# Optimization experiments

Hardware: AMD Instinct MI355X
Metric: run time of the kernel (lower is better)

The kernel has to match this reference:

```python
import jax, jax.numpy as jnp
import numpy as np
import math

D_MODEL = 128
N_HEADS = 8
D_FF = 512
FACTOR = 3
EPS = 1e-5


def _ln(x, g, b):
    mu = x.mean(-1, keepdims=True)
    var = ((x - mu) ** 2).mean(-1, keepdims=True)
    return (x - mu) / jnp.sqrt(var + EPS) * g + b


def setup_inputs() -> dict:
    key = jax.random.key(0)
    ks = jax.random.split(key, 16)
    d, dff = D_MODEL, D_FF
    s = 0.02
    return {
        "x": jax.random.normal(ks[0], (4, 32, 256), dtype=jnp.float32),
        "mlp_w": jax.random.normal(ks[1], (d,)) * s,  # Conv2d(1,d,1x1) weight squeezed
        "mlp_b": jnp.zeros((d,), jnp.float32),
        "wq": jax.random.normal(ks[2], (d, d)) * s, "bq": jnp.zeros((d,), jnp.float32),
        "wk": jax.random.normal(ks[3], (d, d)) * s, "bk": jnp.zeros((d,), jnp.float32),
        "wv": jax.random.normal(ks[4], (d, d)) * s, "bv": jnp.zeros((d,), jnp.float32),
        "wo": jax.random.normal(ks[5], (d, d)) * s, "bo": jnp.zeros((d,), jnp.float32),
        "w1": jax.random.normal(ks[6], (dff, d)) * s, "b1": jnp.zeros((dff,), jnp.float32),
        "w2": jax.random.normal(ks[7], (d, dff)) * s, "b2": jnp.zeros((d,), jnp.float32),
        "ln1_g": jnp.ones((d,), jnp.float32), "ln1_b": jnp.zeros((d,), jnp.float32),
        "ln2_g": jnp.ones((d,), jnp.float32), "ln2_b": jnp.zeros((d,), jnp.float32),
    }


def reference(x, mlp_w, mlp_b, wq, bq, wk, bk, wv, bv, wo, bo,
              w1, b1, w2, b2, ln1_g, ln1_b, ln2_g, ln2_b):
    b, N, T = x.shape
    C, H = D_MODEL, N_HEADS
    E = C // H
    # 1x1 Conv2d from 1 channel -> per-channel affine of scalar input
    h = x[..., None] * mlp_w + mlp_b                      # [b,N,T,C]
    h = h.reshape(b * N, T, C)                            # [B,L,C]
    B, L = h.shape[0], T
    q = (h @ wq.T + bq).reshape(B, L, H, E).transpose(0, 2, 1, 3)  # [B,H,L,E]
    k = (h @ wk.T + bk).reshape(B, L, H, E).transpose(0, 2, 1, 3)
    v = (h @ wv.T + bv).reshape(B, L, H, E).transpose(0, 2, 1, 3)

    sample_k = min(FACTOR * math.ceil(math.log(L)), L)
    u = min(FACTOR * math.ceil(math.log(L)), L)
    # random K-sample indices shared across batch/heads (torch.randint analogue)
    idx = jax.random.randint(jax.random.key(42), (L, sample_k), 0, L)

    scores_full = jnp.einsum('bhle,bhse->bhls', q, k)     # [B,H,L,L]
    qk_sample = jnp.take_along_axis(scores_full, idx[None, None], axis=-1)  # [B,H,L,sample_k]
    M = qk_sample.max(-1) - qk_sample.sum(-1) / L         # sparsity measure
    m_top = jax.lax.top_k(M, u)[1]                        # [B,H,u] top-u query indices
    scores_top = jnp.take_along_axis(scores_full, m_top[..., None], axis=2)  # [B,H,u,L]
    scores_top = scores_top / math.sqrt(E)

    attn = jax.nn.softmax(scores_top, axis=-1)
    upd = jnp.einsum('bhul,bhle->bhue', attn, v)          # [B,H,u,E]
    # mask_flag=False: initial context = mean(V) broadcast over queries
    context = jnp.broadcast_to(v.mean(axis=2, keepdims=True), v.shape)
    bi = jnp.arange(B)[:, None, None]
    hi = jnp.arange(H)[None, :, None]
    context = context.at[bi, hi, m_top].set(upd)          # scatter top-u updates

    out = context.transpose(0, 2, 1, 3).reshape(B, L, C) @ wo.T + bo
    x1 = _ln(h + out, ln1_g, ln1_b)
    y = jax.nn.relu(x1 @ w1.T + b1) @ w2.T + b2           # 1x1 conv1d pair == MLP
    out2 = _ln(x1 + y, ln2_g, ln2_b)
    out2 = out2.reshape(b, N, T, C).sum(axis=1)           # sum over N
    return out2.transpose(0, 2, 1)                        # [b,C,T]
```

## Files before the change

### kernel.cpp

```cpp
#include <hip/hip_runtime.h>
#include <stdint.h>
#include <math.h>


#define EPSF 1e-5f

typedef short bf16x8 __attribute__((ext_vector_type(8)));
typedef float f32x4  __attribute__((ext_vector_type(4)));

__device__ __forceinline__ unsigned short f2bf(float f) {
  union { float f; unsigned u; } v; v.f = f;
  unsigned r = v.u + 0x7FFFu + ((v.u >> 16) & 1u);
  return (unsigned short)(r >> 16);
}
__device__ __forceinline__ float bf2f(unsigned short u) {
  union { unsigned u; float f; } v; v.u = ((unsigned)u) << 16;
  return v.f;
}
__device__ __forceinline__ float waveSum(float v) {
  #pragma unroll
  for (int m = 32; m > 0; m >>= 1) v += __shfl_xor(v, m);
  return v;
}

__device__ __forceinline__ void threefry2x32_k42(uint32_t& x0, uint32_t& x1) {
  const uint32_t ks0 = 0u, ks1 = 42u, ks2 = 0u ^ 42u ^ 0x1BD11BDAu;
  x0 += ks0; x1 += ks1;
#define TF_R(d) { x0 += x1; x1 = (x1 << d) | (x1 >> (32 - d)); x1 ^= x0; }
  TF_R(13) TF_R(15) TF_R(26) TF_R(6)  x0 += ks1; x1 += ks2 + 1u;
  TF_R(17) TF_R(29) TF_R(16) TF_R(24) x0 += ks2; x1 += ks0 + 2u;
  TF_R(13) TF_R(15) TF_R(26) TF_R(6)  x0 += ks0; x1 += ks1 + 3u;
  TF_R(17) TF_R(29) TF_R(16) TF_R(24) x0 += ks1; x1 += ks2 + 4u;
  TF_R(13) TF_R(15) TF_R(26) TF_R(6)  x0 += ks2; x1 += ks0 + 5u;
#undef TF_R
}

__global__ __launch_bounds__(256) void setup_kernel(
    const float* __restrict__ mlp_w, const float* __restrict__ mlp_b,
    const float* __restrict__ wq, const float* __restrict__ bq,
    const float* __restrict__ wk, const float* __restrict__ bk,
    const float* __restrict__ wv, const float* __restrict__ bv,
    const float* __restrict__ wo, const float* __restrict__ bo,
    const float* __restrict__ w1, const float* __restrict__ w2,
    int* __restrict__ idxT, float* __restrict__ cst,
    unsigned short* __restrict__ w1bf, unsigned short* __restrict__ w2bf) {
  int tid = threadIdx.x;
  {
    int gid = blockIdx.x * 256 + tid;
    int base = gid * 16;
    const float* src; unsigned short* dst; int off;
    if (base < 65536) { src = w1; dst = w1bf; off = base; }
    else              { src = w2; dst = w2bf; off = base - 65536; }
    #pragma unroll 4
    for (int k = 0; k < 16; k++) dst[off + k] = f2bf(src[off + k]);
  }
  if (blockIdx.x != 0) return;
  for (int p = tid; p < 2304; p += 256) {
    uint32_t a = (uint32_t)p, bb = (uint32_t)(p + 2304);
    threefry2x32_k42(a, bb);
    int l0 = p / 18, j0 = p - l0 * 18;
    int p2 = p + 2304;
    int l1 = p2 / 18, j1 = p2 - l1 * 18;
    idxT[j0 * 256 + l0] = (int)(a & 0xFFu);
    idxT[j1 * 256 + l1] = (int)(bb & 0xFFu);
  }
  if (tid < 128) {
    float aq = 0.f, cq_ = 0.f, ak = 0.f, ck_ = 0.f, av = 0.f, cv_ = 0.f;
    for (int c = 0; c < 128; c++) {
      float w = mlp_w[c], bb = mlp_b[c];
      float q = wq[tid * 128 + c], k = wk[tid * 128 + c], v = wv[tid * 128 + c];
      aq += q * w; cq_ += q * bb;
      ak += k * w; ck_ += k * bb;
      av += v * w; cv_ += v * bb;
    }
    cst[0   + tid] = aq;
    cst[128 + tid] = cq_ + bq[tid];
    cst[256 + tid] = ak;
    cst[384 + tid] = ck_ + bk[tid];
    cst[512 + tid] = av;
    cst[640 + tid] = cv_ + bv[tid];
  }
  __syncthreads();
  if (tid < 8) {
    float a = 0.f, b = 0.f, g = 0.f, d = 0.f;
    for (int e = 0; e < 16; e++) {
      int j = tid * 16 + e;
      float Aq = cst[j], Cq = cst[128 + j], Ak = cst[256 + j], Ck = cst[384 + j];
      a += Aq * Ak; b += Aq * Ck; g += Cq * Ak; d += Cq * Ck;
    }
    cst[768 + tid] = a; cst[776 + tid] = b; cst[784 + tid] = g; cst[792 + tid] = d;
  }
  if (tid < 128) {
    float oc = 0.f;
    for (int h = 0; h < 8; h++) {
      float s = 0.f;
      for (int e = 0; e < 16; e++) {
        float w = wo[tid * 128 + h * 16 + e];
        s  += w * cst[512 + h * 16 + e];
        oc += w * cst[640 + h * 16 + e];
      }
      cst[800 + h * 128 + tid] = s;
    }
    cst[1824 + tid] = oc + bo[tid] + mlp_b[tid];
  }
}

__global__ __launch_bounds__(256) void attn_kernel(
    const float* __restrict__ x, const int* __restrict__ idxT,
    const float* __restrict__ cst, float* __restrict__ g) {
  __shared__ float xr[256];
  __shared__ float Mb[512];
  __shared__ float selv[512];
  __shared__ float rsum[4], rmax[4], rmin[4];
  __shared__ int   items[64];
  __shared__ float witem[64];
  __shared__ int   cnt;
  int tid = threadIdx.x, lane = tid & 63, w = tid >> 6;
  int seq = blockIdx.x >> 2, hg = blockIdx.x & 3;
  if (tid == 0) cnt = 0;
  float xv = x[seq * 256 + tid];
  xr[tid] = xv;
  float s = waveSum(xv);
  float mx = xv, mn = xv;
  #pragma unroll
  for (int m = 32; m > 0; m >>= 1) {
    mx = fmaxf(mx, __shfl_xor(mx, m));
    mn = fminf(mn, __shfl_xor(mn, m));
  }
  if (lane == 0) { rsum[w] = s; rmax[w] = mx; rmin[w] = mn; }
  __syncthreads();
  float meanx = (rsum[0] + rsum[1] + rsum[2] + rsum[3]) * (1.0f / 256.0f);
  float maxx = fmaxf(fmaxf(rmax[0], rmax[1]), fmaxf(rmax[2], rmax[3]));
  float minx = fminf(fminf(rmin[0], rmin[1]), fminf(rmin[2], rmin[3]));
  float mx18 = -INFINITY, mn18 = INFINITY, s18 = 0.f;
  #pragma unroll 3
  for (int j = 0; j < 18; j++) {
    float xs = xr[idxT[j * 256 + tid]];
    mx18 = fmaxf(mx18, xs); mn18 = fminf(mn18, xs); s18 += xs;
  }
  int h0 = hg * 2, h1 = h0 + 1;
  float al0 = cst[768 + h0], be0 = cst[776 + h0], ga0 = cst[784 + h0], de0 = cst[792 + h0];
  float al1 = cst[768 + h1], be1 = cst[776 + h1], ga1 = cst[784 + h1], de1 = cst[792 + h1];
  float ac0 = fmaf(al0, xv, ga0), cc0 = fmaf(be0, xv, de0);
  float ac1 = fmaf(al1, xv, ga1), cc1 = fmaf(be1, xv, de1);
  float M0 = ((ac0 >= 0.f ? ac0 * mx18 : ac0 * mn18) + cc0)
           - (fmaf(ac0, s18, 18.f * cc0)) * (1.0f / 256.0f);
  float M1 = ((ac1 >= 0.f ? ac1 * mx18 : ac1 * mn18) + cc1)
           - (fmaf(ac1, s18, 18.f * cc1)) * (1.0f / 256.0f);
  Mb[tid] = M0; Mb[256 + tid] = M1;
  __syncthreads();
  int r0 = 0, r1 = 0;
  #pragma unroll 4
  for (int j = 0; j < 256; j++) {
    float a = Mb[j], bb = Mb[256 + j];
    r0 += (a > M0) || (a == M0 && j < tid);
    r1 += (bb > M1) || (bb == M1 && j < tid);
  }
  selv[tid] = meanx; selv[256 + tid] = meanx;
  if (r0 < 18) { int p = atomicAdd(&cnt, 1); items[p] = tid;       witem[p] = 0.25f * ac0; }
  if (r1 < 18) { int p = atomicAdd(&cnt, 1); items[p] = 256 + tid; witem[p] = 0.25f * ac1; }
  __syncthreads();
  int nIt = cnt;
  for (int i = w; i < nIt; i += 4) {
    int it = items[i]; float wv = witem[i];
    float m0 = (wv >= 0.f) ? wv * maxx : wv * minx;
    float S1 = 0.f, Sx = 0.f;
    #pragma unroll
    for (int cch = 0; cch < 4; cch++) {
      float xs = xr[lane + cch * 64];
      float e = __expf(fmaf(wv, xs, -m0));
      S1 += e; Sx = fmaf(xs, e, Sx);
    }
    #pragma unroll
    for (int m = 32; m > 0; m >>= 1) {
      S1 += __shfl_xor(S1, m); Sx += __shfl_xor(Sx, m);
    }
    if (lane == 0) selv[it] = Sx / S1;
  }
  __syncthreads();
  float2 gv; gv.x = selv[tid]; gv.y = selv[256 + tid];
  *(float2*)&g[(size_t)((seq << 8) + tid) * 8 + hg * 2] = gv;
}

__global__ __launch_bounds__(256) void mega_kernel(
    const float* __restrict__ x, const float* __restrict__ g,
    const float* __restrict__ cst, const float* __restrict__ mlp_w,
    const unsigned short* __restrict__ w1bf, const float* __restrict__ b1,
    const unsigned short* __restrict__ w2bf, const float* __restrict__ b2,
    const float* __restrict__ ln1g, const float* __restrict__ ln1b,
    const float* __restrict__ ln2g, const float* __restrict__ ln2b,
    float* __restrict__ out) {
  __shared__ unsigned short x1s[64 * 136];
  __shared__ unsigned short a1s[64 * 264];
  __shared__ float partial[512];
  int tid = threadIdx.x, lane = tid & 63, w = tid >> 6;
  int col = lane & 15, quad = lane >> 4;
  int b = blockIdx.x >> 7, t0 = (blockIdx.x & 127) << 1;

  {
    int c0 = lane << 1;
    float mwa = mlp_w[c0], mwb = mlp_w[c0 | 1];
    float cca = cst[1824 + c0], ccb = cst[1824 + (c0 | 1)];
    float wva[8], wvb[8];
    #pragma unroll
    for (int h = 0; h < 8; h++) {
      wva[h] = cst[800 + h * 128 + c0];
      wvb[h] = cst[800 + h * 128 + (c0 | 1)];
    }
    float g1a = ln1g[c0], g1b = ln1g[c0 | 1];
    float e1a = ln1b[c0], e1b = ln1b[c0 | 1];
    for (int tk = 0; tk < 16; tk++) {
      int row = w * 16 + tk;
      int td = row >> 5, n = row & 31;
      int tok = ((b * 32 + n) << 8) + t0 + td;
      float xvv = x[tok];
      const float* gp = g + (size_t)tok * 8;
      float ra = fmaf(xvv, mwa, cca), rb = fmaf(xvv, mwb, ccb);
      #pragma unroll
      for (int h = 0; h < 8; h++) {
        float gh = gp[h];
        ra = fmaf(gh, wva[h], ra); rb = fmaf(gh, wvb[h], rb);
      }
      float su = waveSum(ra + rb);
      float mu = su * (1.0f / 128.0f);
      float da = ra - mu, db = rb - mu;
      float vs = waveSum(da * da + db * db);
      float inv = rsqrtf(vs * (1.0f / 128.0f) + EPSF);
      unsigned int pa = f2bf(da * inv * g1a + e1a);
      unsigned int pb = f2bf(db * inv * g1b + e1b);
      *(unsigned int*)&x1s[row * 136 + c0] = pa | (pb << 16);
    }
  }
  __syncthreads();

  f32x4 acc2[8];
  #pragma unroll
  for (int i = 0; i < 8; i++) acc2[i] = (f32x4){0.f, 0.f, 0.f, 0.f};

  for (int fh = 0; fh < 2; fh++) {
    f32x4 acc1[16];
    #pragma unroll
    for (int i = 0; i < 16; i++) acc1[i] = (f32x4){0.f, 0.f, 0.f, 0.f};
    #pragma unroll
    for (int ks = 0; ks < 4; ks++) {
      bf16x8 af[4];
      #pragma unroll
      for (int rg = 0; rg < 4; rg++)
        af[rg] = *(const bf16x8*)&x1s[(rg * 16 + col) * 136 + ks * 32 + quad * 8];
      #pragma unroll
      for (int ft = 0; ft < 4; ft++) {
        int f = fh * 256 + w * 64 + ft * 16 + col;
        bf16x8 bf = *(const bf16x8*)(w1bf + f * 128 + ks * 32 + quad * 8);
        #pragma unroll
        for (int rg = 0; rg < 4; rg++)
          acc1[rg * 4 + ft] = __builtin_amdgcn_mfma_f32_16x16x32_bf16(
              af[rg], bf, acc1[rg * 4 + ft], 0, 0, 0);
      }
    }
    if (fh) __syncthreads();
    #pragma unroll
    for (int ft = 0; ft < 4; ft++) {
      int fl = w * 64 + ft * 16 + col;
      float bv = b1[fh * 256 + fl];
      #pragma unroll
      for (int rg = 0; rg < 4; rg++) {
        f32x4 a = acc1[rg * 4 + ft];
        #pragma unroll
        for (int r = 0; r < 4; r++) {
          float vv = fmaxf(a[r] + bv, 0.f);
          a1s[(rg * 16 + quad * 4 + r) * 264 + fl] = f2bf(vv);
        }
      }
    }
    __syncthreads();
    #pragma unroll
    for (int ks = 0; ks < 8; ks++) {
      bf16x8 a2 = *(const bf16x8*)&a1s[(w * 16 + col) * 264 + ks * 32 + quad * 8];
      #pragma unroll
      for (int tc = 0; tc < 8; tc++) {
        int c = tc * 16 + col;
        bf16x8 bf = *(const bf16x8*)(w2bf + c * 512 + fh * 256 + ks * 32 + quad * 8);
        acc2[tc] = __builtin_amdgcn_mfma_f32_16x16x32_bf16(a2, bf, acc2[tc], 0, 0, 0);
      }
    }
  }

  float z[8][4];
  float b2c[8], g2c[8], e2c[8];
  #pragma unroll
  for (int tc = 0; tc < 8; tc++) {
    int c = tc * 16 + col;
    b2c[tc] = b2[c]; g2c[tc] = ln2g[c]; e2c[tc] = ln2b[c];
  }
  #pragma unroll
  for (int tc = 0; tc < 8; tc++)
    #pragma unroll
    for (int r = 0; r < 4; r++) {
      float x1v = bf2f(x1s[(w * 16 + quad * 4 + r) * 136 + tc * 16 + col]);
      z[tc][r] = acc2[tc][r] + b2c[tc] + x1v;
    }
  float mu[4], inv[4];
  #pragma unroll
  for (int r = 0; r < 4; r++) {
    float s = 0.f;
    #pragma unroll
    for (int tc = 0; tc < 8; tc++) s += z[tc][r];
    #pragma unroll
    for (int m = 1; m <= 8; m <<= 1) s += __shfl_xor(s, m);
    mu[r] = s * (1.0f / 128.0f);
  }
  #pragma unroll
  for (int r = 0; r < 4; r++) {
    float q = 0.f;
    #pragma unroll
    for (int tc = 0; tc < 8; tc++) {
      float d = z[tc][r] - mu[r]; q += d * d;
    }
    #pragma unroll
    for (int m = 1; m <= 8; m <<= 1) q += __shfl_xor(q, m);
    inv[r] = rsqrtf(q * (1.0f / 128.0f) + EPSF);
  }
  float nsum[8];
  #pragma unroll
  for (int tc = 0; tc < 8; tc++) {
    float s = 0.f;
    #pragma unroll
    for (int r = 0; r < 4; r++) {
      float o = (z[tc][r] - mu[r]) * inv[r] * g2c[tc] + e2c[tc];
      s += o;
    }
    s += __shfl_xor(s, 16);
    s += __shfl_xor(s, 32);
    nsum[tc] = s;
  }
  if (quad == 0) {
    #pragma unroll
    for (int tc = 0; tc < 8; tc++) partial[w * 128 + tc * 16 + col] = nsum[tc];
  }
  __syncthreads();
  {
    int c = tid & 127, tp = tid >> 7;
    float v = partial[(tp * 2) * 128 + c] + partial[(tp * 2 + 1) * 128 + c];
    out[(size_t)(b * 128 + c) * 256 + t0 + tp] = v;
  }
}

extern "C" void kernel_launch(void* const* d_in, const int* in_sizes, int n_in,
                              void* d_out, int out_size, void* d_ws, size_t ws_size,
                              hipStream_t stream) {
  (void)in_sizes; (void)n_in; (void)out_size; (void)ws_size;
  const float* x    = (const float*)d_in[0];
  const float* mlpw = (const float*)d_in[1];
  const float* mlpb = (const float*)d_in[2];
  const float* wq   = (const float*)d_in[3];
  const float* bq   = (const float*)d_in[4];
  const float* wk   = (const float*)d_in[5];
  const float* bk   = (const float*)d_in[6];
  const float* wv   = (const float*)d_in[7];
  const float* bv   = (const float*)d_in[8];
  const float* wo   = (const float*)d_in[9];
  const float* bo   = (const float*)d_in[10];
  const float* w1   = (const float*)d_in[11];
  const float* b1   = (const float*)d_in[12];
  const float* w2   = (const float*)d_in[13];
  const float* b2   = (const float*)d_in[14];
  const float* ln1g = (const float*)d_in[15];
  const float* ln1b = (const float*)d_in[16];
  const float* ln2g = (const float*)d_in[17];
  const float* ln2b = (const float*)d_in[18];

  char* ws = (char*)d_ws;
  int*            idxT = (int*)(ws);
  float*          cst  = (float*)(ws + 20480);
  unsigned short* w1bf = (unsigned short*)(ws + 32768);
  unsigned short* w2bf = (unsigned short*)(ws + 163840);
  float*          gbuf = (float*)(ws + 294912);
  float*          outp = (float*)d_out;

  hipLaunchKernelGGL(setup_kernel, dim3(32), dim3(256), 0, stream,
                     mlpw, mlpb, wq, bq, wk, bk, wv, bv, wo, bo, w1, w2,
                     idxT, cst, w1bf, w2bf);
  hipLaunchKernelGGL(attn_kernel, dim3(512), dim3(256), 0, stream,
                     x, idxT, cst, gbuf);
  hipLaunchKernelGGL(mega_kernel, dim3(512), dim3(256), 0, stream,
                     x, gbuf, cst, mlpw, w1bf, b1, w2bf, b2,
                     ln1g, ln1b, ln2g, ln2b, outp);
}
```

Measured before the change: 178.5 us.

## Halve mega_kernel tile to 32 rows, restructure LN2 epilogue, refine attn top-k

The MLP mega_kernel now handles one time step (32 rows) per block instead of two, doubling the grid to 1024 blocks. Shared memory is reduced by overlaying a1s with a z buffer, launch bounds request 4 blocks per CU, and the second GEMM is split across waves by output column. LayerNorm2 and the sum over N are redone through shared memory with float4 reads and shuffle reductions. In attn_kernel the rank loop reads Mb as float4, and the softmax pass runs on 32-lane groups using x values preloaded into registers. The extra blocks reload the same weights more often from global memory in exchange for more parallelism and occupancy.

```diff
diff --git a/kernel.cpp b/kernel.cpp
--- a/kernel.cpp
+++ b/kernel.cpp
@@ -132,6 +132,10 @@
   float meanx = (rsum[0] + rsum[1] + rsum[2] + rsum[3]) * (1.0f / 256.0f);
   float maxx = fmaxf(fmaxf(rmax[0], rmax[1]), fmaxf(rmax[2], rmax[3]));
   float minx = fminf(fminf(rmin[0], rmin[1]), fminf(rmin[2], rmin[3]));
+  int l32 = tid & 31, grp = tid >> 5;
+  float xs8[8];
+  #pragma unroll
+  for (int k = 0; k < 8; k++) xs8[k] = xr[l32 + k * 32];
   float mx18 = -INFINITY, mn18 = INFINITY, s18 = 0.f;
   #pragma unroll 3
   for (int j = 0; j < 18; j++) {
@@ -150,39 +154,46 @@
   Mb[tid] = M0; Mb[256 + tid] = M1;
   __syncthreads();
   int r0 = 0, r1 = 0;
+  const float4* Mb4 = (const float4*)Mb;
   #pragma unroll 4
-  for (int j = 0; j < 256; j++) {
-    float a = Mb[j], bb = Mb[256 + j];
-    r0 += (a > M0) || (a == M0 && j < tid);
-    r1 += (bb > M1) || (bb == M1 && j < tid);
+  for (int j4 = 0; j4 < 64; j4++) {
+    float4 a = Mb4[j4], bb = Mb4[64 + j4];
+    int base = j4 * 4;
+    r0 += (a.x > M0) || (a.x == M0 && base     < tid);
+    r0 += (a.y > M0) || (a.y == M0 && base + 1 < tid);
+    r0 += (a.z > M0) || (a.z == M0 && base + 2 < tid);
+    r0 += (a.w > M0) || (a.w == M0 && base + 3 < tid);
+    r1 += (bb.x > M1) || (bb.x == M1 && base     < tid);
+    r1 += (bb.y > M1) || (bb.y == M1 && base + 1 < tid);
+    r1 += (bb.z > M1) || (bb.z == M1 && base + 2 < tid);
+    r1 += (bb.w > M1) || (bb.w == M1 && base + 3 < tid);
   }
   selv[tid] = meanx; selv[256 + tid] = meanx;
   if (r0 < 18) { int p = atomicAdd(&cnt, 1); items[p] = tid;       witem[p] = 0.25f * ac0; }
   if (r1 < 18) { int p = atomicAdd(&cnt, 1); items[p] = 256 + tid; witem[p] = 0.25f * ac1; }
   __syncthreads();
   int nIt = cnt;
-  for (int i = w; i < nIt; i += 4) {
+  for (int i = grp; i < nIt; i += 8) {
     int it = items[i]; float wv = witem[i];
     float m0 = (wv >= 0.f) ? wv * maxx : wv * minx;
     float S1 = 0.f, Sx = 0.f;
     #pragma unroll
-    for (int cch = 0; cch < 4; cch++) {
-      float xs = xr[lane + cch * 64];
-      float e = __expf(fmaf(wv, xs, -m0));
-      S1 += e; Sx = fmaf(xs, e, Sx);
-    }
-    #pragma unroll
-    for (int m = 32; m > 0; m >>= 1) {
+    for (int k = 0; k < 8; k++) {
+      float e = __expf(fmaf(wv, xs8[k], -m0));
+      S1 += e; Sx = fmaf(xs8[k], e, Sx);
+    }
+    #pragma unroll
+    for (int m = 16; m > 0; m >>= 1) {
       S1 += __shfl_xor(S1, m); Sx += __shfl_xor(Sx, m);
     }
-    if (lane == 0) selv[it] = Sx / S1;
+    if (l32 == 0) selv[it] = Sx / S1;
   }
   __syncthreads();
   float2 gv; gv.x = selv[tid]; gv.y = selv[256 + tid];
   *(float2*)&g[(size_t)((seq << 8) + tid) * 8 + hg * 2] = gv;
 }
 
-__global__ __launch_bounds__(256) void mega_kernel(
+__global__ __launch_bounds__(256, 4) void mega_kernel(
     const float* __restrict__ x, const float* __restrict__ g,
     const float* __restrict__ cst, const float* __restrict__ mlp_w,
     const unsigned short* __restrict__ w1bf, const float* __restrict__ b1,
@@ -190,12 +201,14 @@
     const float* __restrict__ ln1g, const float* __restrict__ ln1b,
     const float* __restrict__ ln2g, const float* __restrict__ ln2b,
     float* __restrict__ out) {
-  __shared__ unsigned short x1s[64 * 136];
-  __shared__ unsigned short a1s[64 * 264];
-  __shared__ float partial[512];
+  __shared__ unsigned short x1s[32 * 136];
+  __shared__ char ovl[32 * 264 * 2];
+  __shared__ float psum[512];
+  unsigned short* a1s = (unsigned short*)ovl;
+  float*          zbuf = (float*)ovl;
   int tid = threadIdx.x, lane = tid & 63, w = tid >> 6;
   int col = lane & 15, quad = lane >> 4;
-  int b = blockIdx.x >> 7, t0 = (blockIdx.x & 127) << 1;
+  int b = blockIdx.x >> 8, t = blockIdx.x & 255;
 
   {
     int c0 = lane << 1;
@@ -209,18 +222,21 @@
     }
     float g1a = ln1g[c0], g1b = ln1g[c0 | 1];
     float e1a = ln1b[c0], e1b = ln1b[c0 | 1];
-    for (int tk = 0; tk < 16; tk++) {
-      int row = w * 16 + tk;
-      int td = row >> 5, n = row & 31;
-      int tok = ((b * 32 + n) << 8) + t0 + td;
+    for (int tk = 0; tk < 8; tk++) {
+      int n = w * 8 + tk;
+      int tok = ((b * 32 + n) << 8) + t;
       float xvv = x[tok];
-      const float* gp = g + (size_t)tok * 8;
+      float4 gA = *(const float4*)(g + (size_t)tok * 8);
+      float4 gB = *(const float4*)(g + (size_t)tok * 8 + 4);
       float ra = fmaf(xvv, mwa, cca), rb = fmaf(xvv, mwb, ccb);
-      #pragma unroll
-      for (int h = 0; h < 8; h++) {
-        float gh = gp[h];
-        ra = fmaf(gh, wva[h], ra); rb = fmaf(gh, wvb[h], rb);
-      }
+      ra = fmaf(gA.x, wva[0], ra); rb = fmaf(gA.x, wvb[0], rb);
+      ra = fmaf(gA.y, wva[1], ra); rb = fmaf(gA.y, wvb[1], rb);
+      ra = fmaf(gA.z, wva[2], ra); rb = fmaf(gA.z, wvb[2], rb);
+      ra = fmaf(gA.w, wva[3], ra); rb = fmaf(gA.w, wvb[3], rb);
+      ra = fmaf(gB.x, wva[4], ra); rb = fmaf(gB.x, wvb[4], rb);
+      ra = fmaf(gB.y, wva[5], ra); rb = fmaf(gB.y, wvb[5], rb);
+      ra = fmaf(gB.z, wva[6], ra); rb = fmaf(gB.z, wvb[6], rb);
+      ra = fmaf(gB.w, wva[7], ra); rb = fmaf(gB.w, wvb[7], rb);
       float su = waveSum(ra + rb);
       float mu = su * (1.0f / 128.0f);
       float da = ra - mu, db = rb - mu;
@@ -228,33 +244,33 @@
       float inv = rsqrtf(vs * (1.0f / 128.0f) + EPSF);
       unsigned int pa = f2bf(da * inv * g1a + e1a);
       unsigned int pb = f2bf(db * inv * g1b + e1b);
-      *(unsigned int*)&x1s[row * 136 + c0] = pa | (pb << 16);
-    }
-  }
-  __syncthreads();
-
-  f32x4 acc2[8];
+      *(unsigned int*)&x1s[n * 136 + c0] = pa | (pb << 16);
+    }
+  }
+  __syncthreads();
+
+  f32x4 acc2[4];
   #pragma unroll
-  for (int i = 0; i < 8; i++) acc2[i] = (f32x4){0.f, 0.f, 0.f, 0.f};
+  for (int i = 0; i < 4; i++) acc2[i] = (f32x4){0.f, 0.f, 0.f, 0.f};
 
   for (int fh = 0; fh < 2; fh++) {
-    f32x4 acc1[16];
-    #pragma unroll
-    for (int i = 0; i < 16; i++) acc1[i] = (f32x4){0.f, 0.f, 0.f, 0.f};
+    f32x4 acc1[8];
+    #pragma unroll
+    for (int i = 0; i < 8; i++) acc1[i] = (f32x4){0.f, 0.f, 0.f, 0.f};
     #pragma unroll
     for (int ks = 0; ks < 4; ks++) {
-      bf16x8 af[4];
-      #pragma unroll
-      for (int rg = 0; rg < 4; rg++)
+      bf16x8 af[2];
+      #pragma unroll
+      for (int rg = 0; rg < 2; rg++)
         af[rg] = *(const bf16x8*)&x1s[(rg * 16 + col) * 136 + ks * 32 + quad * 8];
       #pragma unroll
       for (int ft = 0; ft < 4; ft++) {
         int f = fh * 256 + w * 64 + ft * 16 + col;
-        bf16x8 bf = *(const bf16x8*)(w1bf + f * 128 + ks * 32 + quad * 8);
+        bf16x8 bfr = *(const bf16x8*)(w1bf + f * 128 + ks * 32 + quad * 8);
         #pragma unroll
-        for (int rg = 0; rg < 4; rg++)
+        for (int rg = 0; rg < 2; rg++)
           acc1[rg * 4 + ft] = __builtin_amdgcn_mfma_f32_16x16x32_bf16(
-              af[rg], bf, acc1[rg * 4 + ft], 0, 0, 0);
+              af[rg], bfr, acc1[rg * 4 + ft], 0, 0, 0);
       }
     }
     if (fh) __syncthreads();
@@ -263,7 +279,7 @@
       int fl = w * 64 + ft * 16 + col;
       float bv = b1[fh * 256 + fl];
       #pragma unroll
-      for (int rg = 0; rg < 4; rg++) {
+      for (int rg = 0; rg < 2; rg++) {
         f32x4 a = acc1[rg * 4 + ft];
         #pragma unroll
         for (int r = 0; r < 4; r++) {
@@ -275,73 +291,90 @@
     __syncthreads();
     #pragma unroll
     for (int ks = 0; ks < 8; ks++) {
-      bf16x8 a2 = *(const bf16x8*)&a1s[(w * 16 + col) * 264 + ks * 32 + quad * 8];
-      #pragma unroll
-      for (int tc = 0; tc < 8; tc++) {
-        int c = tc * 16 + col;
-        bf16x8 bf = *(const bf16x8*)(w2bf + c * 512 + fh * 256 + ks * 32 + quad * 8);
-        acc2[tc] = __builtin_amdgcn_mfma_f32_16x16x32_bf16(a2, bf, acc2[tc], 0, 0, 0);
-      }
-    }
-  }
-
-  float z[8][4];
-  float b2c[8], g2c[8], e2c[8];
+      bf16x8 a2[2];
+      #pragma unroll
+      for (int rg = 0; rg < 2; rg++)
+        a2[rg] = *(const bf16x8*)&a1s[(rg * 16 + col) * 264 + ks * 32 + quad * 8];
+      #pragma unroll
+      for (int tc = 0; tc < 2; tc++) {
+        int c = w * 32 + tc * 16 + col;
+        bf16x8 bfr = *(const bf16x8*)(w2bf + c * 512 + fh * 256 + ks * 32 + quad * 8);
+        #pragma unroll
+        for (int rg = 0; rg < 2; rg++)
+          acc2[rg * 2 + tc] = __builtin_amdgcn_mfma_f32_16x16x32_bf16(
+              a2[rg], bfr, acc2[rg * 2 + tc], 0, 0, 0);
+      }
+    }
+  }
+  __syncthreads();
+
   #pragma unroll
-  for (int tc = 0; tc < 8; tc++) {
-    int c = tc * 16 + col;
-    b2c[tc] = b2[c]; g2c[tc] = ln2g[c]; e2c[tc] = ln2b[c];
-  }
-  #pragma unroll
-  for (int tc = 0; tc < 8; tc++)
-    #pragma unroll
-    for (int r = 0; r < 4; r++) {
-      float x1v = bf2f(x1s[(w * 16 + quad * 4 + r) * 136 + tc * 16 + col]);
-      z[tc][r] = acc2[tc][r] + b2c[tc] + x1v;
-    }
-  float mu[4], inv[4];
-  #pragma unroll
-  for (int r = 0; r < 4; r++) {
+  for (int tc = 0; tc < 2; tc++) {
+    int c = w * 32 + tc * 16 + col;
+    float b2c = b2[c];
+    #pragma unroll
+    for (int rg = 0; rg < 2; rg++) {
+      #pragma unroll
+      for (int r = 0; r < 4; r++) {
+        int row = rg * 16 + quad * 4 + r;
+        float z = acc2[rg * 2 + tc][r] + b2c + bf2f(x1s[row * 136 + c]);
+        zbuf[row * 132 + c] = z;
+      }
+    }
+  }
+  __syncthreads();
+
+  {
+    int rloc = lane & 7, part = lane >> 3;
+    int row = w * 8 + rloc;
+    float4 zv[4];
+    #pragma unroll
+    for (int q = 0; q < 4; q++)
+      zv[q] = *(const float4*)&zbuf[row * 132 + part * 16 + q * 4];
     float s = 0.f;
     #pragma unroll
-    for (int tc = 0; tc < 8; tc++) s += z[tc][r];
-    #pragma unroll
-    for (int m = 1; m <= 8; m <<= 1) s += __shfl_xor(s, m);
-    mu[r] = s * (1.0f / 128.0f);
-  }
-  #pragma unroll
-  for (int r = 0; r < 4; r++) {
-    float q = 0.f;
-    #pragma unroll
-    for (int tc = 0; tc < 8; tc++) {
-      float d = z[tc][r] - mu[r]; q += d * d;
-    }
-    #pragma unroll
-    for (int m = 1; m <= 8; m <<= 1) q += __shfl_xor(q, m);
-    inv[r] = rsqrtf(q * (1.0f / 128.0f) + EPSF);
-  }
-  float nsum[8];
-  #pragma unroll
-  for (int tc = 0; tc < 8; tc++) {
-    float s = 0.f;
-    #pragma unroll
-    for (int r = 0; r < 4; r++) {
-      float o = (z[tc][r] - mu[r]) * inv[r] * g2c[tc] + e2c[tc];
-      s += o;
-    }
-    s += __shfl_xor(s, 16);
-    s += __shfl_xor(s, 32);
-    nsum[tc] = s;
-  }
-  if (quad == 0) {
-    #pragma unroll
-    for (int tc = 0; tc < 8; tc++) partial[w * 128 + tc * 16 + col] = nsum[tc];
-  }
-  __syncthreads();
-  {
-    int c = tid & 127, tp = tid >> 7;
-    float v = partial[(tp * 2) * 128 + c] + partial[(tp * 2 + 1) * 128 + c];
-    out[(size_t)(b * 128 + c) * 256 + t0 + tp] = v;
+    for (int q = 0; q < 4; q++) s += zv[q].x + zv[q].y + zv[q].z + zv[q].w;
+    s += __shfl_xor(s, 8); s += __shfl_xor(s, 16); s += __shfl_xor(s, 32);
+    float mu = s * (1.0f / 128.0f);
+    float ss = 0.f;
+    #pragma unroll
+    for (int q = 0; q < 4; q++) {
+      float d0 = zv[q].x - mu, d1 = zv[q].y - mu, d2 = zv[q].z - mu, d3 = zv[q].w - mu;
+      ss += d0 * d0 + d1 * d1 + d2 * d2 + d3 * d3;
+    }
+    ss += __shfl_xor(ss, 8); ss += __shfl_xor(ss, 16); ss += __shfl_xor(ss, 32);
+    float inv = rsqrtf(ss * (1.0f / 128.0f) + EPSF);
+    float4 o[4];
+    #pragma unroll
+    for (int q = 0; q < 4; q++) {
+      float4 g2v = *(const float4*)(ln2g + part * 16 + q * 4);
+      float4 e2v = *(const float4*)(ln2b + part * 16 + q * 4);
+      o[q].x = (zv[q].x - mu) * inv * g2v.x + e2v.x;
+      o[q].y = (zv[q].y - mu) * inv * g2v.y + e2v.y;
+      o[q].z = (zv[q].z - mu) * inv * g2v.z + e2v.z;
+      o[q].w = (zv[q].w - mu) * inv * g2v.w + e2v.w;
+    }
+    #pragma unroll
+    for (int m = 1; m <= 4; m <<= 1) {
+      #pragma unroll
+      for (int q = 0; q < 4; q++) {
+        o[q].x += __shfl_xor(o[q].x, m);
+        o[q].y += __shfl_xor(o[q].y, m);
+        o[q].z += __shfl_xor(o[q].z, m);
+        o[q].w += __shfl_xor(o[q].w, m);
+      }
+    }
+    if (rloc == 0) {
+      #pragma unroll
+      for (int q = 0; q < 4; q++)
+        *(float4*)&psum[w * 128 + part * 16 + q * 4] = o[q];
+    }
+  }
+  __syncthreads();
+  if (tid < 128) {
+    int c = tid;
+    float v = psum[c] + psum[128 + c] + psum[256 + c] + psum[384 + c];
+    out[(size_t)(b * 128 + c) * 256 + t] = v;
   }
 }
 
@@ -382,7 +415,7 @@
                      idxT, cst, w1bf, w2bf);
   hipLaunchKernelGGL(attn_kernel, dim3(512), dim3(256), 0, stream,
                      x, idxT, cst, gbuf);
-  hipLaunchKernelGGL(mega_kernel, dim3(512), dim3(256), 0, stream,
+  hipLaunchKernelGGL(mega_kernel, dim3(1024), dim3(256), 0, stream,
                      x, gbuf, cst, mlpw, w1bf, b1, w2bf, b2,
                      ln1g, ln1b, ln2g, ln2b, outp);
 }
```

After: 163.7 us. 8.3% less time.
